# Optimization experiments

Measured on AMD Instinct MI355X. Metric: run time of the kernel, lower is better.

## Reference

```python
import jax, jax.numpy as jnp
import numpy as np

K = 16  # number of piecewise-linear intervals (fixed in params_set)


def setup_inputs() -> dict:
    key = jax.random.key(0)
    k1, k2 = jax.random.split(key)
    B, S, D = 4, 4096, 2048
    x = jax.random.normal(k1, (B, S, D), dtype=jnp.float32)
    threshold = jnp.ones((1,), dtype=jnp.float32)          # alpha > 0
    theta = 0.1 * jax.random.normal(k2, (K,), dtype=jnp.float32)
    dst = jnp.arange(K, dtype=jnp.float32) / K             # delta * arange(K), delta = 1/K
    return {
        "x": x,
        "threshold": threshold,
        "theta": theta,
        "dst": dst,
        "Qn": 0,
        "Qp": 15,                 # 2**4 - 1 (activation, num_bits=4)
        "num_elements": B * S * D,
    }


def reference(x, threshold, theta, dst, Qn, Qp, num_elements):
    # LCQ_quantizer.forward (non 2-bit-weight path) -> LCQ_fast_core.forward
    s = float(Qp)
    theta_tmp = jax.nn.softmax(theta)                       # softmax over dim 0
    gamma = theta_tmp * K                                   # theta_tmp / delta
    beta = jnp.concatenate(
        [jnp.zeros((1,), theta_tmp.dtype), jnp.cumsum(theta_tmp)[: K - 1]]
    )
    alpha = threshold                                       # shape (1,), broadcasts

    flag_middle = (jnp.abs(x) < alpha).astype(x.dtype)
    flag_high = 1.0 - flag_middle
    x_tmp = jnp.abs(x) / alpha

    # compress: searchsorted bin lookup + piecewise affine
    idx = jnp.searchsorted(dst, x_tmp, side="right")        # in [1, K]
    y = gamma[idx - 1] * (x_tmp - dst[idx - 1]) + beta[idx - 1]
    y_q = jnp.round(y * s) / s                              # uniform round-quantize

    # expand: second searchsorted + inverse affine
    idx_q = jnp.searchsorted(beta, y_q, side="right")       # in [1, K]
    z_mid = (y_q - beta[idx_q - 1]) / gamma[idx_q - 1] + dst[idx_q - 1]

    z = jnp.sign(x) * alpha * (z_mid * flag_middle + flag_high)
    return z
```

## Files before the change

### kernel.cpp

```cpp
#include <hip/hip_runtime.h>
#include <math.h>

#define KB 16

typedef float vf4 __attribute__((ext_vector_type(4)));

__device__ __forceinline__ float lcq_core(float xv, float alpha, float rcp_alpha,
                                          const float2* __restrict__ s_gb,
                                          const float* __restrict__ s_zval)
{
    float a   = fabsf(xv);
    float xt  = __fmul_rn(a, rcp_alpha);
    float t16 = __fmul_rn(xt, 16.0f);
    float jf  = fminf(t16, 15.0f);
    int   j   = (int)jf;
    float2 gb = s_gb[j];
    float dj  = __fmul_rn(floorf(jf), 0.0625f);
    float y   = __fadd_rn(__fmul_rn(gb.x, __fsub_rn(xt, dj)), gb.y);
    float t   = rintf(__fmul_rn(y, 15.0f));
    int   m   = (int)fminf(t, 15.0f);
    float v   = (a < alpha) ? s_zval[m] : 1.0f;
    float r   = __fmul_rn(alpha, v);
    return copysignf(r, xv);
}

__global__ __launch_bounds__(256) void lcq_kernel(
    const float* __restrict__ x,
    const float* __restrict__ thr,
    const float* __restrict__ theta,
    float* __restrict__ out,
    long long n)
{
    __shared__ float2 s_gb[KB];
    __shared__ float  s_zval[KB];
    __shared__ float  s_scal[2];

    if (threadIdx.x == 0) {
        float th[KB];
        float mx = theta[0];
        th[0] = mx;
        #pragma unroll
        for (int i = 1; i < KB; ++i) { th[i] = theta[i]; mx = fmaxf(mx, th[i]); }
        float ex[KB];
        float sum = 0.0f;
        #pragma unroll
        for (int i = 0; i < KB; ++i) { ex[i] = expf(__fsub_rn(th[i], mx)); sum = __fadd_rn(sum, ex[i]); }
        float sm[KB];
        #pragma unroll
        for (int i = 0; i < KB; ++i) sm[i] = __fdiv_rn(ex[i], sum);

        float beta[KB], gamma[KB];
        beta[0] = 0.0f;
        float c = sm[0];
        #pragma unroll
        for (int i = 1; i < KB; ++i) { beta[i] = c; c = __fadd_rn(c, sm[i]); }
        #pragma unroll
        for (int i = 0; i < KB; ++i) gamma[i] = __fmul_rn(sm[i], 16.0f);

        #pragma unroll
        for (int i = 0; i < KB; ++i) s_gb[i] = make_float2(gamma[i], beta[i]);

        for (int m = 0; m < KB; ++m) {
            float yq = __fdiv_rn((float)m, 15.0f);
            int iq = 0;
            #pragma unroll
            for (int i = 1; i < KB; ++i) iq += (beta[i] <= yq) ? 1 : 0;
            s_zval[m] = __fadd_rn(__fdiv_rn(__fsub_rn(yq, beta[iq]), gamma[iq]),
                                  (float)iq * 0.0625f);
        }
        float alpha = thr[0];
        s_scal[0] = alpha;
        s_scal[1] = __fdiv_rn(1.0f, alpha);
    }
    __syncthreads();

    const float alpha = s_scal[0];
    const float rcpa  = s_scal[1];

    const long long n4ll = n >> 2;
    const vf4* __restrict__ x4 = (const vf4*)x;
    vf4* __restrict__ o4 = (vf4*)out;

    const unsigned base = blockIdx.x * 1024u + threadIdx.x;

    if ((long long)(blockIdx.x + 1) * 1024ll <= n4ll) {
        vf4 v0 = x4[base];
        vf4 v1 = x4[base + 256u];
        vf4 v2 = x4[base + 512u];
        vf4 v3 = x4[base + 768u];
        vf4 r0, r1, r2, r3;
        r0.x = lcq_core(v0.x, alpha, rcpa, s_gb, s_zval);
        r0.y = lcq_core(v0.y, alpha, rcpa, s_gb, s_zval);
        r0.z = lcq_core(v0.z, alpha, rcpa, s_gb, s_zval);
        r0.w = lcq_core(v0.w, alpha, rcpa, s_gb, s_zval);
        r1.x = lcq_core(v1.x, alpha, rcpa, s_gb, s_zval);
        r1.y = lcq_core(v1.y, alpha, rcpa, s_gb, s_zval);
        r1.z = lcq_core(v1.z, alpha, rcpa, s_gb, s_zval);
        r1.w = lcq_core(v1.w, alpha, rcpa, s_gb, s_zval);
        r2.x = lcq_core(v2.x, alpha, rcpa, s_gb, s_zval);
        r2.y = lcq_core(v2.y, alpha, rcpa, s_gb, s_zval);
        r2.z = lcq_core(v2.z, alpha, rcpa, s_gb, s_zval);
        r2.w = lcq_core(v2.w, alpha, rcpa, s_gb, s_zval);
        r3.x = lcq_core(v3.x, alpha, rcpa, s_gb, s_zval);
        r3.y = lcq_core(v3.y, alpha, rcpa, s_gb, s_zval);
        r3.z = lcq_core(v3.z, alpha, rcpa, s_gb, s_zval);
        r3.w = lcq_core(v3.w, alpha, rcpa, s_gb, s_zval);
        o4[base]        = r0;
        o4[base + 256u] = r1;
        o4[base + 512u] = r2;
        o4[base + 768u] = r3;
    } else {
        #pragma unroll
        for (int k = 0; k < 4; ++k) {
            long long i = (long long)base + k * 256;
            if (i < n4ll) {
                vf4 v = x4[i];
                vf4 r;
                r.x = lcq_core(v.x, alpha, rcpa, s_gb, s_zval);
                r.y = lcq_core(v.y, alpha, rcpa, s_gb, s_zval);
                r.z = lcq_core(v.z, alpha, rcpa, s_gb, s_zval);
                r.w = lcq_core(v.w, alpha, rcpa, s_gb, s_zval);
                o4[i] = r;
            }
        }
        if (blockIdx.x == gridDim.x - 1) {
            for (long long k = (n4ll << 2) + threadIdx.x; k < n; k += 256) {
                out[k] = lcq_core(x[k], alpha, rcpa, s_gb, s_zval);
            }
        }
    }
}

extern "C" void kernel_launch(void* const* d_in, const int* in_sizes, int n_in,
                              void* d_out, int out_size, void* d_ws, size_t ws_size,
                              hipStream_t stream) {
    const float* x     = (const float*)d_in[0];
    const float* thr   = (const float*)d_in[1];
    const float* theta = (const float*)d_in[2];
    float* out = (float*)d_out;

    long long n = (long long)in_sizes[0];
    long long n4 = n >> 2;
    long long grid = (n4 + 1023) / 1024;
    if (grid < 1) grid = 1;
    dim3 block(256);
    hipLaunchKernelGGL(lcq_kernel, dim3((unsigned)grid), block, 0, stream,
                       x, thr, theta, out, n);
}
```

Before: 243.5 us.

## Process four chunks per block with double-buffered loads and nontemporal stores

Each block now handles 4096 float4 vectors instead of 1024, software-pipelining loads of the next chunk while the current one is computed, and writes output with nontemporal stores. The per-block table setup (softmax, cumsum, zval table) is amortised over four times more data, and alpha is folded into the lookup table to drop one multiply per element. The cost is a quarter as many blocks, which lowers parallelism, and more registers held live across chunks.

```diff
diff --git a/kernel.cpp b/kernel.cpp
--- a/kernel.cpp
+++ b/kernel.cpp
@@ -7,7 +7,7 @@
 
 __device__ __forceinline__ float lcq_core(float xv, float alpha, float rcp_alpha,
                                           const float2* __restrict__ s_gb,
-                                          const float* __restrict__ s_zval)
+                                          const float* __restrict__ s_pv)
 {
     float a   = fabsf(xv);
     float xt  = __fmul_rn(a, rcp_alpha);
@@ -19,8 +19,7 @@
     float y   = __fadd_rn(__fmul_rn(gb.x, __fsub_rn(xt, dj)), gb.y);
     float t   = rintf(__fmul_rn(y, 15.0f));
     int   m   = (int)fminf(t, 15.0f);
-    float v   = (a < alpha) ? s_zval[m] : 1.0f;
-    float r   = __fmul_rn(alpha, v);
+    float r   = (a < alpha) ? s_pv[m] : alpha;
     return copysignf(r, xv);
 }
 
@@ -32,7 +31,7 @@
     long long n)
 {
     __shared__ float2 s_gb[KB];
-    __shared__ float  s_zval[KB];
+    __shared__ float  s_pv[KB];
     __shared__ float  s_scal[2];
 
     if (threadIdx.x == 0) {
@@ -60,17 +59,19 @@
         #pragma unroll
         for (int i = 0; i < KB; ++i) s_gb[i] = make_float2(gamma[i], beta[i]);
 
+        float alpha = thr[0];
+        s_scal[0] = alpha;
+        s_scal[1] = __fdiv_rn(1.0f, alpha);
+
         for (int m = 0; m < KB; ++m) {
             float yq = __fdiv_rn((float)m, 15.0f);
             int iq = 0;
             #pragma unroll
             for (int i = 1; i < KB; ++i) iq += (beta[i] <= yq) ? 1 : 0;
-            s_zval[m] = __fadd_rn(__fdiv_rn(__fsub_rn(yq, beta[iq]), gamma[iq]),
-                                  (float)iq * 0.0625f);
+            float zv = __fadd_rn(__fdiv_rn(__fsub_rn(yq, beta[iq]), gamma[iq]),
+                                 (float)iq * 0.0625f);
+            s_pv[m] = __fmul_rn(alpha, zv);
         }
-        float alpha = thr[0];
-        s_scal[0] = alpha;
-        s_scal[1] = __fdiv_rn(1.0f, alpha);
     }
     __syncthreads();
 
@@ -81,54 +82,71 @@
     const vf4* __restrict__ x4 = (const vf4*)x;
     vf4* __restrict__ o4 = (vf4*)out;
 
-    const unsigned base = blockIdx.x * 1024u + threadIdx.x;
+    const size_t blk = (size_t)blockIdx.x * 4096u + threadIdx.x;
 
-    if ((long long)(blockIdx.x + 1) * 1024ll <= n4ll) {
-        vf4 v0 = x4[base];
-        vf4 v1 = x4[base + 256u];
-        vf4 v2 = x4[base + 512u];
-        vf4 v3 = x4[base + 768u];
-        vf4 r0, r1, r2, r3;
-        r0.x = lcq_core(v0.x, alpha, rcpa, s_gb, s_zval);
-        r0.y = lcq_core(v0.y, alpha, rcpa, s_gb, s_zval);
-        r0.z = lcq_core(v0.z, alpha, rcpa, s_gb, s_zval);
-        r0.w = lcq_core(v0.w, alpha, rcpa, s_gb, s_zval);
-        r1.x = lcq_core(v1.x, alpha, rcpa, s_gb, s_zval);
-        r1.y = lcq_core(v1.y, alpha, rcpa, s_gb, s_zval);
-        r1.z = lcq_core(v1.z, alpha, rcpa, s_gb, s_zval);
-        r1.w = lcq_core(v1.w, alpha, rcpa, s_gb, s_zval);
-        r2.x = lcq_core(v2.x, alpha, rcpa, s_gb, s_zval);
-        r2.y = lcq_core(v2.y, alpha, rcpa, s_gb, s_zval);
-        r2.z = lcq_core(v2.z, alpha, rcpa, s_gb, s_zval);
-        r2.w = lcq_core(v2.w, alpha, rcpa, s_gb, s_zval);
-        r3.x = lcq_core(v3.x, alpha, rcpa, s_gb, s_zval);
-        r3.y = lcq_core(v3.y, alpha, rcpa, s_gb, s_zval);
-        r3.z = lcq_core(v3.z, alpha, rcpa, s_gb, s_zval);
-        r3.w = lcq_core(v3.w, alpha, rcpa, s_gb, s_zval);
-        o4[base]        = r0;
-        o4[base + 256u] = r1;
-        o4[base + 512u] = r2;
-        o4[base + 768u] = r3;
+#define LCQ_LOAD(V0, V1, V2, V3, off) \
+    V0 = x4[blk + (off)];        V1 = x4[blk + (off) + 256u]; \
+    V2 = x4[blk + (off) + 512u]; V3 = x4[blk + (off) + 768u];
+
+#define LCQ_CS(V0, V1, V2, V3, off) { \
+    vf4 r0, r1, r2, r3; \
+    r0.x = lcq_core(V0.x, alpha, rcpa, s_gb, s_pv); \
+    r0.y = lcq_core(V0.y, alpha, rcpa, s_gb, s_pv); \
+    r0.z = lcq_core(V0.z, alpha, rcpa, s_gb, s_pv); \
+    r0.w = lcq_core(V0.w, alpha, rcpa, s_gb, s_pv); \
+    r1.x = lcq_core(V1.x, alpha, rcpa, s_gb, s_pv); \
+    r1.y = lcq_core(V1.y, alpha, rcpa, s_gb, s_pv); \
+    r1.z = lcq_core(V1.z, alpha, rcpa, s_gb, s_pv); \
+    r1.w = lcq_core(V1.w, alpha, rcpa, s_gb, s_pv); \
+    r2.x = lcq_core(V2.x, alpha, rcpa, s_gb, s_pv); \
+    r2.y = lcq_core(V2.y, alpha, rcpa, s_gb, s_pv); \
+    r2.z = lcq_core(V2.z, alpha, rcpa, s_gb, s_pv); \
+    r2.w = lcq_core(V2.w, alpha, rcpa, s_gb, s_pv); \
+    r3.x = lcq_core(V3.x, alpha, rcpa, s_gb, s_pv); \
+    r3.y = lcq_core(V3.y, alpha, rcpa, s_gb, s_pv); \
+    r3.z = lcq_core(V3.z, alpha, rcpa, s_gb, s_pv); \
+    r3.w = lcq_core(V3.w, alpha, rcpa, s_gb, s_pv); \
+    __builtin_nontemporal_store(r0, (vf4*)&o4[blk + (off)]); \
+    __builtin_nontemporal_store(r1, (vf4*)&o4[blk + (off) + 256u]); \
+    __builtin_nontemporal_store(r2, (vf4*)&o4[blk + (off) + 512u]); \
+    __builtin_nontemporal_store(r3, (vf4*)&o4[blk + (off) + 768u]); }
+
+    if ((long long)(blockIdx.x + 1) * 4096ll <= n4ll) {
+        vf4 a0, a1, a2, a3;
+        vf4 b0, b1, b2, b3;
+        LCQ_LOAD(a0, a1, a2, a3, 0u)
+        LCQ_LOAD(b0, b1, b2, b3, 1024u)
+        LCQ_CS(a0, a1, a2, a3, 0u)
+        LCQ_LOAD(a0, a1, a2, a3, 2048u)
+        LCQ_CS(b0, b1, b2, b3, 1024u)
+        LCQ_LOAD(b0, b1, b2, b3, 3072u)
+        LCQ_CS(a0, a1, a2, a3, 2048u)
+        LCQ_CS(b0, b1, b2, b3, 3072u)
     } else {
-        #pragma unroll
-        for (int k = 0; k < 4; ++k) {
-            long long i = (long long)base + k * 256;
-            if (i < n4ll) {
-                vf4 v = x4[i];
-                vf4 r;
-                r.x = lcq_core(v.x, alpha, rcpa, s_gb, s_zval);
-                r.y = lcq_core(v.y, alpha, rcpa, s_gb, s_zval);
-                r.z = lcq_core(v.z, alpha, rcpa, s_gb, s_zval);
-                r.w = lcq_core(v.w, alpha, rcpa, s_gb, s_zval);
-                o4[i] = r;
+        #pragma unroll 1
+        for (int c = 0; c < 4; ++c) {
+            #pragma unroll
+            for (int k = 0; k < 4; ++k) {
+                long long i = (long long)blk + c * 1024 + k * 256;
+                if (i < n4ll) {
+                    vf4 v = x4[i];
+                    vf4 r;
+                    r.x = lcq_core(v.x, alpha, rcpa, s_gb, s_pv);
+                    r.y = lcq_core(v.y, alpha, rcpa, s_gb, s_pv);
+                    r.z = lcq_core(v.z, alpha, rcpa, s_gb, s_pv);
+                    r.w = lcq_core(v.w, alpha, rcpa, s_gb, s_pv);
+                    o4[i] = r;
+                }
             }
         }
         if (blockIdx.x == gridDim.x - 1) {
             for (long long k = (n4ll << 2) + threadIdx.x; k < n; k += 256) {
-                out[k] = lcq_core(x[k], alpha, rcpa, s_gb, s_zval);
+                out[k] = lcq_core(x[k], alpha, rcpa, s_gb, s_pv);
             }
         }
     }
+#undef LCQ_LOAD
+#undef LCQ_CS
 }
 
 extern "C" void kernel_launch(void* const* d_in, const int* in_sizes, int n_in,
@@ -141,7 +159,8 @@
 
     long long n = (long long)in_sizes[0];
     long long n4 = n >> 2;
-    long long grid = (n4 + 1023) / 1024;
+    long long chunks = (n4 + 1023) / 1024;
+    long long grid = (chunks + 3) / 4;
     if (grid < 1) grid = 1;
     dim3 block(256);
     hipLaunchKernelGGL(lcq_kernel, dim3((unsigned)grid), block, 0, stream,
```

Result: slower. 253.8 us (+4.2%).
